# Kernel tuning notes

Hardware: AMD Instinct MI355X
Metric: run time of the kernel (lower is better)

## Reference

```python
import jax, jax.numpy as jnp
import numpy as np

N_ITEMS = 100000
EMBED_DIM = 64
N_REL = 3
N_EDGES = 3200000


def setup_inputs() -> dict:
    key = jax.random.key(0)
    k1, k2, k3, k4 = jax.random.split(key, 4)
    item_embeddings = jax.random.normal(k1, (N_ITEMS, EMBED_DIM), dtype=jnp.float32)
    rows = jax.random.randint(k2, (N_REL, N_EDGES), 0, N_ITEMS, dtype=jnp.int64)
    cols = jax.random.randint(k3, (N_REL, N_EDGES), 0, N_ITEMS, dtype=jnp.int64)
    vals = jax.random.uniform(k4, (N_REL, N_EDGES), dtype=jnp.float32)
    return {"item_embeddings": item_embeddings, "rows": rows, "cols": cols, "vals": vals}


def reference(item_embeddings, rows, cols, vals):
    # item_embeddings: [N, D]; rows/cols/vals: [R, E] COO edge lists per relation.
    n_items, _ = item_embeddings.shape
    n_rel = rows.shape[0]
    rel_emb = jnp.zeros_like(item_embeddings)
    for r in range(n_rel):  # fixed small number of relation types
        # SpMM: neighbor_emb[i] = sum_{e: rows[e]==i} vals[e] * E[cols[e]]
        msgs = item_embeddings[cols[r]] * vals[r][:, None]          # [E, D]
        neighbor = jax.ops.segment_sum(msgs, rows[r], num_segments=n_items)  # [N, D]
        # degree = row sum of adjacency values, clamped to min 1
        degree = jax.ops.segment_sum(vals[r], rows[r], num_segments=n_items)  # [N]
        degree = jnp.maximum(degree, 1.0)
        rel_emb = rel_emb + neighbor / degree[:, None]
    rel_emb = rel_emb / n_rel
    return item_embeddings + rel_emb
```

## Files before the change

kernel.cpp:

```cpp
#include <hip/hip_runtime.h>

#define N_ITEMS     100000
#define EMBED_DIM   64
#define N_REL       3
#define N_EDGES     3200000
#define TOTAL_EDGES (N_REL * N_EDGES)
#define NKEY        (N_REL * N_ITEMS)

#define LOG_CH   6
#define CH_ROWS  64
#define NCHUNK   1563
#define NBKT     (NCHUNK * N_REL)
#define BCAP     2368
#define LOG_CB   12
#define NCB      25
#define TILEP    4096
#define SEGSB    34
#define CBCAP    (SEGSB * TILEP)
#define NTILEA   ((N_EDGES + TILEP - 1) / TILEP)

__global__ void initall_kernel(unsigned* __restrict__ gcursorF,
                               unsigned* __restrict__ cursorC) {
    int i = blockIdx.x * 256 + threadIdx.x;
    if (i < NBKT) gcursorF[i] = (unsigned)i * (unsigned)BCAP;
    if (i < N_REL * NCB) cursorC[i] = (unsigned)(i % NCB) * (unsigned)CBCAP;
}

__global__ void tobf16_kernel(const float* __restrict__ E, unsigned short* __restrict__ Ebf) {
    int i = blockIdx.x * 256 + threadIdx.x;
    if (i < N_ITEMS * EMBED_DIM) {
        unsigned u = __float_as_uint(E[i]);
        unsigned r = (u + 0x7FFFu + ((u >> 16) & 1u)) >> 16;
        Ebf[i] = (unsigned short)r;
    }
}

__launch_bounds__(512)
__global__ void partA_kernel(const int* __restrict__ rows,
                             const int* __restrict__ cols,
                             const float* __restrict__ vals,
                             unsigned* __restrict__ cursorC,
                             uint2* __restrict__ coarse,
                             int rel) {
    __shared__ uint2 stag[TILEP];
    __shared__ unsigned char bkt[TILEP];
    __shared__ unsigned hist[NCB], lstart[NCB], gbase[NCB], lcur[NCB];
    int base = blockIdx.x * TILEP;
    int cnt = N_EDGES - base; if (cnt > TILEP) cnt = TILEP;
    int t = threadIdx.x;
    const int go = rel * N_EDGES + base;

    if (t < NCB) hist[t] = 0u;
    __syncthreads();
    for (int i = t; i < cnt; i += 512)
        atomicAdd(&hist[(unsigned)rows[go + i] >> LOG_CB], 1u);
    __syncthreads();
    if (t == 0) {
        unsigned run = 0;
        for (int j = 0; j < NCB; j++) { unsigned v = hist[j]; lstart[j] = run; lcur[j] = run; run += v; }
    }
    __syncthreads();
    if (t < NCB && hist[t]) gbase[t] = atomicAdd(&cursorC[rel * NCB + t], hist[t]);
    __syncthreads();
    for (int i = t; i < cnt; i += 512) {
        unsigned row = (unsigned)rows[go + i];
        unsigned cb = row >> LOG_CB;
        unsigned dst = atomicAdd(&lcur[cb], 1u);
        stag[dst] = make_uint2((unsigned)cols[go + i] | ((row & 4095u) << 17),
                               __float_as_uint(vals[go + i]));
        bkt[dst] = (unsigned char)cb;
    }
    __syncthreads();
    for (int i = t; i < cnt; i += 512) {
        unsigned bb = bkt[i];
        unsigned dst = gbase[bb] + ((unsigned)i - lstart[bb]);
        if (dst < (bb + 1u) * (unsigned)CBCAP) coarse[dst] = stag[i];
    }
}

__launch_bounds__(512)
__global__ void partB_kernel(const unsigned* __restrict__ cursorC,
                             const uint2* __restrict__ coarse,
                             unsigned* __restrict__ gcursorF,
                             uint2* __restrict__ recs,
                             int rel) {
    __shared__ uint2 stag[TILEP];
    __shared__ unsigned char bkt[TILEP];
    __shared__ unsigned hist[64], lstart[64], gbase[64], lcur[64];
    int cb = blockIdx.x / SEGSB, seg = blockIdx.x % SEGSB;
    unsigned cntA = cursorC[rel * NCB + cb] - (unsigned)cb * (unsigned)CBCAP;
    if (cntA > (unsigned)CBCAP) cntA = (unsigned)CBCAP;
    int off = seg * TILEP;
    int cnt = (int)cntA - off;
    if (cnt <= 0) return;
    if (cnt > TILEP) cnt = TILEP;
    const uint2* __restrict__ src = coarse + (unsigned)cb * (unsigned)CBCAP + off;
    int t = threadIdx.x;

    if (t < 64) hist[t] = 0u;
    __syncthreads();
    for (int i = t; i < cnt; i += 512)
        atomicAdd(&hist[(src[i].x >> 23) & 63u], 1u);
    __syncthreads();
    if (t == 0) {
        unsigned run = 0;
        for (int j = 0; j < 64; j++) { unsigned v = hist[j]; lstart[j] = run; lcur[j] = run; run += v; }
    }
    __syncthreads();
    if (t < 64 && hist[t])
        gbase[t] = atomicAdd(&gcursorF[(((unsigned)cb << 6) + t) * 3u + rel], hist[t]);
    __syncthreads();
    for (int i = t; i < cnt; i += 512) {
        uint2 rc = src[i];
        unsigned j = (rc.x >> 23) & 63u;
        unsigned dst = atomicAdd(&lcur[j], 1u);
        stag[dst] = make_uint2(rc.x & 0x7FFFFFu, rc.y);
        bkt[dst] = (unsigned char)j;
    }
    __syncthreads();
    for (int i = t; i < cnt; i += 512) {
        unsigned j = bkt[i];
        unsigned bf = (((unsigned)cb << 6) + j) * 3u + rel;
        unsigned dst = gbase[j] + ((unsigned)i - lstart[j]);
        if (dst < (bf + 1u) * (unsigned)BCAP) recs[dst] = stag[i];
    }
}

__launch_bounds__(512, 8)
__global__ void gather_sort_kernel(const uint2* __restrict__ Ebf4,
                                   const float* __restrict__ E,
                                   const unsigned* __restrict__ gcursorF,
                                   const uint2* __restrict__ recs,
                                   float* __restrict__ out) {
    __shared__ uint2  srt[BCAP];
    __shared__ float4 accT4[CH_ROWS * 16];
    __shared__ unsigned hist[CH_ROWS], cur[CH_ROWS], rstart[CH_ROWS + 1];
    int c = blockIdx.x;
    int t = threadIdx.x;
    int w = t >> 6;
    int lane = t & 63;
    int sub = lane >> 4;
    int q = lane & 15;

    float* accT = (float*)accT4;
    for (int k = t; k < CH_ROWS * EMBED_DIM; k += 512) accT[k] = 0.f;

    for (int rel = 0; rel < N_REL; rel++) {
        unsigned b = (unsigned)(c * N_REL + rel);
        unsigned s0 = b * (unsigned)BCAP;
        int n = (int)(gcursorF[b] - s0);
        if (n > BCAP) n = BCAP;
        const uint2* __restrict__ pg = recs + s0;

        uint2 rc[5];
        #pragma unroll
        for (int k = 0; k < 5; k++) {
            int i = t + (k << 9);
            rc[k] = (i < n) ? pg[i] : make_uint2(0u, 0u);
        }
        if (t < CH_ROWS) hist[t] = 0u;
        __syncthreads();
        #pragma unroll
        for (int k = 0; k < 5; k++) {
            int i = t + (k << 9);
            if (i < n) atomicAdd(&hist[rc[k].x >> 17], 1u);
        }
        __syncthreads();
        if (t < 64) {
            unsigned v = hist[t];
            unsigned inc = v;
            #pragma unroll
            for (int d = 1; d < 64; d <<= 1) {
                unsigned x = __shfl_up(inc, d, 64);
                if (lane >= d) inc += x;
            }
            rstart[t] = inc - v;
            cur[t] = inc - v;
            if (t == 63) rstart[64] = inc;
        }
        __syncthreads();
        #pragma unroll
        for (int k = 0; k < 5; k++) {
            int i = t + (k << 9);
            if (i < n) {
                unsigned pos = atomicAdd(&cur[rc[k].x >> 17], 1u);
                srt[pos] = make_uint2(rc[k].x & 0x1FFFFu, rc[k].y);
            }
        }
        __syncthreads();

        for (int k = 0; k < 8; k++) {
            int r = (w << 3) + k;
            int base = (int)rstart[r];
            int nr = (int)(rstart[r + 1] - rstart[r]);
            float a0 = 0.f, a1 = 0.f, a2 = 0.f, a3 = 0.f, dg = 0.f;
            int i = sub;
            for (; i + 12 < nr; i += 16) {
                uint2 r0 = srt[base + i],     r1 = srt[base + i + 4];
                uint2 r2 = srt[base + i + 8], r3 = srt[base + i + 12];
                uint2 e0 = Ebf4[r0.x * 16u + q];
                uint2 e1 = Ebf4[r1.x * 16u + q];
                uint2 e2 = Ebf4[r2.x * 16u + q];
                uint2 e3 = Ebf4[r3.x * 16u + q];
                float w0 = __uint_as_float(r0.y), w1 = __uint_as_float(r1.y);
                float w2 = __uint_as_float(r2.y), w3 = __uint_as_float(r3.y);
                a0 += w0 * __uint_as_float(e0.x << 16);
                a1 += w0 * __uint_as_float(e0.x & 0xFFFF0000u);
                a2 += w0 * __uint_as_float(e0.y << 16);
                a3 += w0 * __uint_as_float(e0.y & 0xFFFF0000u);
                dg += w0;
                a0 += w1 * __uint_as_float(e1.x << 16);
                a1 += w1 * __uint_as_float(e1.x & 0xFFFF0000u);
                a2 += w1 * __uint_as_float(e1.y << 16);
                a3 += w1 * __uint_as_float(e1.y & 0xFFFF0000u);
                dg += w1;
                a0 += w2 * __uint_as_float(e2.x << 16);
                a1 += w2 * __uint_as_float(e2.x & 0xFFFF0000u);
                a2 += w2 * __uint_as_float(e2.y << 16);
                a3 += w2 * __uint_as_float(e2.y & 0xFFFF0000u);
                dg += w2;
                a0 += w3 * __uint_as_float(e3.x << 16);
                a1 += w3 * __uint_as_float(e3.x & 0xFFFF0000u);
                a2 += w3 * __uint_as_float(e3.y << 16);
                a3 += w3 * __uint_as_float(e3.y & 0xFFFF0000u);
                dg += w3;
            }
            for (; i < nr; i += 4) {
                uint2 r0 = srt[base + i];
                uint2 e0 = Ebf4[r0.x * 16u + q];
                float w0 = __uint_as_float(r0.y);
                a0 += w0 * __uint_as_float(e0.x << 16);
                a1 += w0 * __uint_as_float(e0.x & 0xFFFF0000u);
                a2 += w0 * __uint_as_float(e0.y << 16);
                a3 += w0 * __uint_as_float(e0.y & 0xFFFF0000u);
                dg += w0;
            }
            a0 += __shfl_xor(a0, 16, 64);  a0 += __shfl_xor(a0, 32, 64);
            a1 += __shfl_xor(a1, 16, 64);  a1 += __shfl_xor(a1, 32, 64);
            a2 += __shfl_xor(a2, 16, 64);  a2 += __shfl_xor(a2, 32, 64);
            a3 += __shfl_xor(a3, 16, 64);  a3 += __shfl_xor(a3, 32, 64);
            dg += __shfl_xor(dg, 16, 64);  dg += __shfl_xor(dg, 32, 64);
            float inv = 1.0f / (3.0f * fmaxf(dg, 1.0f));
            if (sub == 0) {
                float4 o = accT4[(r << 4) + q];
                accT4[(r << 4) + q] = make_float4(o.x + a0 * inv, o.y + a1 * inv,
                                                  o.z + a2 * inv, o.w + a3 * inv);
            }
        }
        __syncthreads();
    }

    int gbase2 = c * (CH_ROWS * EMBED_DIM);
    for (int k = t; k < CH_ROWS * EMBED_DIM; k += 512) {
        int gi = gbase2 + k;
        if (gi < N_ITEMS * EMBED_DIM) out[gi] = E[gi] + accT[k];
    }
}

__global__ void binscatter_cap_kernel(const int* __restrict__ rows,
                                      const int* __restrict__ cols,
                                      const float* __restrict__ vals,
                                      unsigned* __restrict__ gcursor,
                                      uint2* __restrict__ recs) {
    int stride = gridDim.x * blockDim.x;
    for (int i = blockIdx.x * blockDim.x + threadIdx.x; i < TOTAL_EDGES; i += stride) {
        unsigned rel = (unsigned)i / (unsigned)N_EDGES;
        unsigned row = (unsigned)rows[i];
        unsigned b = (row >> LOG_CH) * 3u + rel;
        unsigned pos = atomicAdd(&gcursor[b], 1u);
        if (pos < (b + 1u) * (unsigned)BCAP)
            recs[pos] = make_uint2((unsigned)cols[i] | ((row & (unsigned)(CH_ROWS - 1)) << 17),
                                   __float_as_uint(vals[i]));
    }
}

#define NBS ((NKEY + 255) / 256)

__global__ void hist300_kernel(const int* __restrict__ rows, unsigned* __restrict__ cnt) {
    int stride = gridDim.x * blockDim.x;
    for (int i = blockIdx.x * blockDim.x + threadIdx.x; i < TOTAL_EDGES; i += stride) {
        unsigned r = (unsigned)i / (unsigned)N_EDGES;
        unsigned key = r * N_ITEMS + (unsigned)rows[i];
        atomicAdd(&cnt[key], 1u);
    }
}

__global__ void scan_blocksum(const unsigned* __restrict__ cnt, unsigned* __restrict__ bsum) {
    __shared__ unsigned s[256];
    int i = blockIdx.x * 256 + threadIdx.x;
    s[threadIdx.x] = (i < NKEY) ? cnt[i] : 0u;
    __syncthreads();
    for (int off = 128; off > 0; off >>= 1) {
        if (threadIdx.x < off) s[threadIdx.x] += s[threadIdx.x + off];
        __syncthreads();
    }
    if (threadIdx.x == 0) bsum[blockIdx.x] = s[0];
}

__global__ void scan_partials(unsigned* __restrict__ bsum, unsigned* __restrict__ starts) {
    const int IT = 5;
    int t = threadIdx.x;
    unsigned loc[IT];
    unsigned sum = 0;
    #pragma unroll
    for (int k = 0; k < IT; k++) {
        int idx = t * IT + k;
        loc[k] = (idx < NBS) ? bsum[idx] : 0u;
        sum += loc[k];
    }
    int lane = t & 63, wid = t >> 6;
    unsigned inc = sum;
    #pragma unroll
    for (int d = 1; d < 64; d <<= 1) {
        unsigned x = __shfl_up(inc, d, 64);
        if (lane >= d) inc += x;
    }
    __shared__ unsigned woff[4], woffEx[4];
    if (lane == 63) woff[wid] = inc;
    __syncthreads();
    if (t == 0) { unsigned run = 0; for (int k = 0; k < 4; k++) { woffEx[k] = run; run += woff[k]; } }
    __syncthreads();
    unsigned ex = inc - sum + woffEx[wid];
    #pragma unroll
    for (int k = 0; k < IT; k++) {
        int idx = t * IT + k;
        if (idx < NBS) { bsum[idx] = ex; ex += loc[k]; }
    }
    if (t == 0) starts[NKEY] = (unsigned)TOTAL_EDGES;
}

__global__ void scan_final(unsigned* key_arr,
                           const unsigned* __restrict__ bsum,
                           unsigned* __restrict__ cursor) {
    int i = blockIdx.x * 256 + threadIdx.x;
    unsigned v = (i < NKEY) ? key_arr[i] : 0u;
    int lane = threadIdx.x & 63, wid = threadIdx.x >> 6;
    unsigned inc = v;
    #pragma unroll
    for (int d = 1; d < 64; d <<= 1) {
        unsigned x = __shfl_up(inc, d, 64);
        if (lane >= d) inc += x;
    }
    __shared__ unsigned woff[4], woffEx[4];
    if (lane == 63) woff[wid] = inc;
    __syncthreads();
    if (threadIdx.x == 0) { unsigned run = 0; for (int k = 0; k < 4; k++) { woffEx[k] = run; run += woff[k]; } }
    __syncthreads();
    unsigned ex = inc - v + woffEx[wid] + bsum[blockIdx.x];
    if (i < NKEY) { key_arr[i] = ex; cursor[i] = ex; }
}

__global__ void binscatter2_kernel(const int* __restrict__ rows,
                                   const int* __restrict__ cols,
                                   const float* __restrict__ vals,
                                   unsigned* __restrict__ cursor,
                                   uint2* __restrict__ recs) {
    int stride = gridDim.x * blockDim.x;
    for (int i = blockIdx.x * blockDim.x + threadIdx.x; i < TOTAL_EDGES; i += stride) {
        unsigned r = (unsigned)i / (unsigned)N_EDGES;
        unsigned key = r * N_ITEMS + (unsigned)rows[i];
        unsigned pos = atomicAdd(&cursor[key], 1u);
        uint2 rec;
        rec.x = (unsigned)cols[i];
        rec.y = __float_as_uint(vals[i]);
        recs[pos] = rec;
    }
}

__launch_bounds__(192)
__global__ void gather_csr_f32_kernel(const float* __restrict__ E,
                                      const unsigned* __restrict__ starts,
                                      const uint2* __restrict__ recs,
                                      float* __restrict__ out) {
    __shared__ float part[N_REL * EMBED_DIM];
    int row = blockIdx.x;
    int w = threadIdx.x >> 6;
    int d = threadIdx.x & 63;
    unsigned key = (unsigned)w * N_ITEMS + (unsigned)row;
    unsigned s = starts[key];
    int n = (int)(starts[key + 1] - s);
    const uint2* __restrict__ p = recs + s;
    float acc = 0.0f, deg = 0.0f;
    int j = 0;
    for (; j + 8 <= n; j += 8) {
        uint2 a[8];
        #pragma unroll
        for (int k = 0; k < 8; k++) a[k] = p[j + k];
        float e[8];
        #pragma unroll
        for (int k = 0; k < 8; k++) e[k] = E[a[k].x * EMBED_DIM + d];
        #pragma unroll
        for (int k = 0; k < 8; k++) {
            float wv = __uint_as_float(a[k].y);
            acc += wv * e[k];
            deg += wv;
        }
    }
    for (; j < n; j++) {
        uint2 a = p[j];
        float wv = __uint_as_float(a.y);
        acc += wv * E[a.x * EMBED_DIM + d];
        deg += wv;
    }
    part[w * EMBED_DIM + d] = acc / (3.0f * fmaxf(deg, 1.0f));
    __syncthreads();
    if (threadIdx.x < EMBED_DIM) {
        int gi = row * EMBED_DIM + threadIdx.x;
        out[gi] = E[gi] + part[threadIdx.x]
                        + part[EMBED_DIM + threadIdx.x]
                        + part[2 * EMBED_DIM + threadIdx.x];
    }
}

__global__ void deg_kernel(const int* __restrict__ rows,
                           const float* __restrict__ vals,
                           float* __restrict__ deg) {
    long long i = (long long)blockIdx.x * blockDim.x + threadIdx.x;
    if (i >= TOTAL_EDGES) return;
    int r = (int)(i / N_EDGES);
    int row = rows[i];
    atomicAdd(&deg[(long long)r * N_ITEMS + row], vals[i]);
}

__global__ void inv_kernel(float* __restrict__ deg) {
    int i = blockIdx.x * blockDim.x + threadIdx.x;
    if (i >= N_REL * N_ITEMS) return;
    float d = deg[i];
    d = fmaxf(d, 1.0f);
    deg[i] = 1.0f / (3.0f * d);
}

__global__ void scatter_kernel(const float* __restrict__ E,
                               const int* __restrict__ rows,
                               const int* __restrict__ cols,
                               const float* __restrict__ vals,
                               const float* __restrict__ inv,
                               float* __restrict__ out) {
    long long t = (long long)blockIdx.x * blockDim.x + threadIdx.x;
    long long edge = t >> 6;
    int d = (int)(t & 63);
    if (edge >= TOTAL_EDGES) return;
    int r = (int)(edge / N_EDGES);
    int row = rows[edge];
    int col = cols[edge];
    float w = vals[edge] * inv[r * N_ITEMS + row];
    float msg = w * E[(long long)col * EMBED_DIM + d];
    atomicAdd(&out[(long long)row * EMBED_DIM + d], msg);
}

extern "C" void kernel_launch(void* const* d_in, const int* in_sizes, int n_in,
                              void* d_out, int out_size, void* d_ws, size_t ws_size,
                              hipStream_t stream) {
    const float* E    = (const float*)d_in[0];
    const int*   rows = (const int*)d_in[1];
    const int*   cols = (const int*)d_in[2];
    const float* vals = (const float*)d_in[3];
    float* out = (float*)d_out;

    const size_t GCB      = 32768;
    const size_t COARSE_B = (size_t)NCB * CBCAP * sizeof(uint2);
    const size_t FINE_B   = (size_t)NBKT * BCAP * sizeof(uint2);
    const size_t EBF_B    = (size_t)N_ITEMS * EMBED_DIM * 2;
    size_t need11 = GCB + COARSE_B + FINE_B + EBF_B;
    size_t need10 = GCB + FINE_B + EBF_B;

    const size_t REGA = 1204224;
    const size_t REGC = 8192;
    const size_t RECB = (size_t)TOTAL_EDGES * sizeof(uint2);
    size_t need5 = 2 * REGA + REGC + RECB;

    if (ws_size >= need11) {
        unsigned* gcursorF = (unsigned*)d_ws;
        unsigned* cursorC  = (unsigned*)((char*)d_ws + 20480);
        uint2*    coarse   = (uint2*)((char*)d_ws + GCB);
        uint2*    recs     = (uint2*)((char*)d_ws + GCB + COARSE_B);
        unsigned short* Ebf = (unsigned short*)((char*)d_ws + GCB + COARSE_B + FINE_B);

        initall_kernel<<<(NBKT + 255) / 256, 256, 0, stream>>>(gcursorF, cursorC);
        tobf16_kernel<<<(N_ITEMS * EMBED_DIM + 255) / 256, 256, 0, stream>>>(E, Ebf);
        for (int r = 0; r < N_REL; r++) {
            partA_kernel<<<NTILEA, 512, 0, stream>>>(rows, cols, vals, cursorC, coarse, r);
            partB_kernel<<<NCB * SEGSB, 512, 0, stream>>>(cursorC, coarse, gcursorF, recs, r);
        }
        gather_sort_kernel<<<NCHUNK, 512, 0, stream>>>((const uint2*)Ebf, E, gcursorF, recs, out);
    } else if (ws_size >= need10) {
        unsigned* gcursorF = (unsigned*)d_ws;
        unsigned* cursorC  = (unsigned*)((char*)d_ws + 20480);
        uint2*    recs     = (uint2*)((char*)d_ws + GCB);
        unsigned short* Ebf = (unsigned short*)((char*)d_ws + GCB + FINE_B);

        initall_kernel<<<(NBKT + 255) / 256, 256, 0, stream>>>(gcursorF, cursorC);
        tobf16_kernel<<<(N_ITEMS * EMBED_DIM + 255) / 256, 256, 0, stream>>>(E, Ebf);
        binscatter_cap_kernel<<<2048, 256, 0, stream>>>(rows, cols, vals, gcursorF, recs);
        gather_sort_kernel<<<NCHUNK, 512, 0, stream>>>((const uint2*)Ebf, E, gcursorF, recs, out);
    } else if (ws_size >= need5) {
        unsigned* keyA   = (unsigned*)d_ws;
        unsigned* cursor = (unsigned*)((char*)d_ws + REGA);
        unsigned* bsum   = (unsigned*)((char*)d_ws + 2 * REGA);
        uint2*    recs   = (uint2*)((char*)d_ws + 2 * REGA + REGC);

        hipMemsetAsync(keyA, 0, NKEY * sizeof(unsigned), stream);
        hist300_kernel<<<1536, 256, 0, stream>>>(rows, keyA);
        scan_blocksum<<<NBS, 256, 0, stream>>>(keyA, bsum);
        scan_partials<<<1, 256, 0, stream>>>(bsum, keyA);
        scan_final<<<NBS, 256, 0, stream>>>(keyA, bsum, cursor);
        binscatter2_kernel<<<2048, 256, 0, stream>>>(rows, cols, vals, cursor, recs);
        gather_csr_f32_kernel<<<N_ITEMS, 192, 0, stream>>>(E, keyA, recs, out);
    } else {
        float* deg = (float*)d_ws;
        hipMemsetAsync(deg, 0, (size_t)N_REL * N_ITEMS * sizeof(float), stream);
        {
            long long total = TOTAL_EDGES;
            int block = 256;
            long long grid = (total + block - 1) / block;
            deg_kernel<<<(unsigned)grid, block, 0, stream>>>(rows, vals, deg);
        }
        {
            int total = N_REL * N_ITEMS;
            int block = 256;
            int grid = (total + block - 1) / block;
            inv_kernel<<<grid, block, 0, stream>>>(deg);
        }
        hipMemcpyAsync(out, E, (size_t)N_ITEMS * EMBED_DIM * sizeof(float),
                       hipMemcpyDeviceToDevice, stream);
        {
            long long threads = (long long)TOTAL_EDGES * 64;
            int block = 256;
            long long grid = (threads + block - 1) / block;
            scatter_kernel<<<(unsigned)grid, block, 0, stream>>>(E, rows, cols, vals, deg, out);
        }
    }
}
```

Measured before the change: 440.1 us.

## Batch all relations into single partition launches with register-staged edges and warp scans

Adds per-relation coarse buffers so both partition passes run all three relations in one launch each, replacing six serialized launches with two. It halves the tile size so each thread holds its edges in registers, loading them once instead of twice. The serial single-thread prefix scan over bucket histograms is replaced by a wavefront shuffle scan. In exchange the workspace need grows by two more coarse buffers, and a fallback path keeps the per-relation loop when workspace is too small.

```diff
diff --git a/kernel.cpp b/kernel.cpp
--- a/kernel.cpp
+++ b/kernel.cpp
@@ -14,10 +14,10 @@
 #define BCAP     2368
 #define LOG_CB   12
 #define NCB      25
-#define TILEP    4096
-#define SEGSB    34
+#define TILEP    2048
+#define NTILEP   ((N_EDGES + TILEP - 1) / TILEP)
+#define SEGSB    68
 #define CBCAP    (SEGSB * TILEP)
-#define NTILEA   ((N_EDGES + TILEP - 1) / TILEP)
 
 __global__ void initall_kernel(unsigned* __restrict__ gcursorF,
                                unsigned* __restrict__ cursorC) {
@@ -36,87 +36,125 @@
 }
 
 __launch_bounds__(512)
-__global__ void partA_kernel(const int* __restrict__ rows,
-                             const int* __restrict__ cols,
-                             const float* __restrict__ vals,
-                             unsigned* __restrict__ cursorC,
-                             uint2* __restrict__ coarse,
-                             int rel) {
+__global__ void partA2_kernel(const int* __restrict__ rows,
+                              const int* __restrict__ cols,
+                              const float* __restrict__ vals,
+                              unsigned* __restrict__ cursorC,
+                              uint2* __restrict__ coarse,
+                              int rel0, unsigned relStrideU2) {
     __shared__ uint2 stag[TILEP];
     __shared__ unsigned char bkt[TILEP];
     __shared__ unsigned hist[NCB], lstart[NCB], gbase[NCB], lcur[NCB];
-    int base = blockIdx.x * TILEP;
+    int rel = rel0 + blockIdx.x / NTILEP;
+    int base = (blockIdx.x % NTILEP) * TILEP;
     int cnt = N_EDGES - base; if (cnt > TILEP) cnt = TILEP;
     int t = threadIdx.x;
     const int go = rel * N_EDGES + base;
-
+    uint2* __restrict__ coarseRel = coarse + (size_t)(rel - rel0) * relStrideU2;
+
+    unsigned rrow[4], rcol[4], rval[4];
+    #pragma unroll
+    for (int k = 0; k < 4; k++) {
+        int i = t + (k << 9);
+        if (i < cnt) {
+            rrow[k] = (unsigned)rows[go + i];
+            rcol[k] = (unsigned)cols[go + i];
+            rval[k] = __float_as_uint(vals[go + i]);
+        } else rrow[k] = 0xFFFFFFFFu;
+    }
     if (t < NCB) hist[t] = 0u;
     __syncthreads();
-    for (int i = t; i < cnt; i += 512)
-        atomicAdd(&hist[(unsigned)rows[go + i] >> LOG_CB], 1u);
-    __syncthreads();
-    if (t == 0) {
-        unsigned run = 0;
-        for (int j = 0; j < NCB; j++) { unsigned v = hist[j]; lstart[j] = run; lcur[j] = run; run += v; }
-    }
-    __syncthreads();
-    if (t < NCB && hist[t]) gbase[t] = atomicAdd(&cursorC[rel * NCB + t], hist[t]);
-    __syncthreads();
-    for (int i = t; i < cnt; i += 512) {
-        unsigned row = (unsigned)rows[go + i];
-        unsigned cb = row >> LOG_CB;
-        unsigned dst = atomicAdd(&lcur[cb], 1u);
-        stag[dst] = make_uint2((unsigned)cols[go + i] | ((row & 4095u) << 17),
-                               __float_as_uint(vals[go + i]));
-        bkt[dst] = (unsigned char)cb;
-    }
+    #pragma unroll
+    for (int k = 0; k < 4; k++)
+        if (rrow[k] != 0xFFFFFFFFu) atomicAdd(&hist[rrow[k] >> LOG_CB], 1u);
+    __syncthreads();
+    if (t < 32) {
+        unsigned v = (t < NCB) ? hist[t] : 0u;
+        unsigned inc = v;
+        #pragma unroll
+        for (int d = 1; d < 32; d <<= 1) {
+            unsigned x = __shfl_up(inc, d, 32);
+            if (t >= d) inc += x;
+        }
+        if (t < NCB) {
+            unsigned ex = inc - v;
+            lstart[t] = ex; lcur[t] = ex;
+            if (v) gbase[t] = atomicAdd(&cursorC[rel * NCB + t], v);
+        }
+    }
+    __syncthreads();
+    #pragma unroll
+    for (int k = 0; k < 4; k++)
+        if (rrow[k] != 0xFFFFFFFFu) {
+            unsigned row = rrow[k];
+            unsigned cb = row >> LOG_CB;
+            unsigned dst = atomicAdd(&lcur[cb], 1u);
+            stag[dst] = make_uint2(rcol[k] | ((row & 4095u) << 17), rval[k]);
+            bkt[dst] = (unsigned char)cb;
+        }
     __syncthreads();
     for (int i = t; i < cnt; i += 512) {
         unsigned bb = bkt[i];
         unsigned dst = gbase[bb] + ((unsigned)i - lstart[bb]);
-        if (dst < (bb + 1u) * (unsigned)CBCAP) coarse[dst] = stag[i];
+        if (dst < (bb + 1u) * (unsigned)CBCAP) coarseRel[dst] = stag[i];
     }
 }
 
 __launch_bounds__(512)
-__global__ void partB_kernel(const unsigned* __restrict__ cursorC,
-                             const uint2* __restrict__ coarse,
-                             unsigned* __restrict__ gcursorF,
-                             uint2* __restrict__ recs,
-                             int rel) {
+__global__ void partB2_kernel(const unsigned* __restrict__ cursorC,
+                              const uint2* __restrict__ coarse,
+                              unsigned* __restrict__ gcursorF,
+                              uint2* __restrict__ recs,
+                              int rel0, unsigned relStrideU2) {
     __shared__ uint2 stag[TILEP];
     __shared__ unsigned char bkt[TILEP];
     __shared__ unsigned hist[64], lstart[64], gbase[64], lcur[64];
-    int cb = blockIdx.x / SEGSB, seg = blockIdx.x % SEGSB;
+    int rel = rel0 + blockIdx.x / (NCB * SEGSB);
+    int rem = blockIdx.x % (NCB * SEGSB);
+    int cb = rem / SEGSB, seg = rem % SEGSB;
     unsigned cntA = cursorC[rel * NCB + cb] - (unsigned)cb * (unsigned)CBCAP;
     if (cntA > (unsigned)CBCAP) cntA = (unsigned)CBCAP;
     int off = seg * TILEP;
     int cnt = (int)cntA - off;
     if (cnt <= 0) return;
     if (cnt > TILEP) cnt = TILEP;
-    const uint2* __restrict__ src = coarse + (unsigned)cb * (unsigned)CBCAP + off;
+    const uint2* __restrict__ src = coarse + (size_t)(rel - rel0) * relStrideU2
+                                  + (unsigned)cb * (unsigned)CBCAP + off;
     int t = threadIdx.x;
 
+    uint2 rc[4];
+    #pragma unroll
+    for (int k = 0; k < 4; k++) {
+        int i = t + (k << 9);
+        rc[k] = (i < cnt) ? src[i] : make_uint2(0xFFFFFFFFu, 0u);
+    }
     if (t < 64) hist[t] = 0u;
     __syncthreads();
-    for (int i = t; i < cnt; i += 512)
-        atomicAdd(&hist[(src[i].x >> 23) & 63u], 1u);
-    __syncthreads();
-    if (t == 0) {
-        unsigned run = 0;
-        for (int j = 0; j < 64; j++) { unsigned v = hist[j]; lstart[j] = run; lcur[j] = run; run += v; }
-    }
-    __syncthreads();
-    if (t < 64 && hist[t])
-        gbase[t] = atomicAdd(&gcursorF[(((unsigned)cb << 6) + t) * 3u + rel], hist[t]);
-    __syncthreads();
-    for (int i = t; i < cnt; i += 512) {
-        uint2 rc = src[i];
-        unsigned j = (rc.x >> 23) & 63u;
-        unsigned dst = atomicAdd(&lcur[j], 1u);
-        stag[dst] = make_uint2(rc.x & 0x7FFFFFu, rc.y);
-        bkt[dst] = (unsigned char)j;
-    }
+    #pragma unroll
+    for (int k = 0; k < 4; k++)
+        if (rc[k].x != 0xFFFFFFFFu) atomicAdd(&hist[(rc[k].x >> 23) & 63u], 1u);
+    __syncthreads();
+    if (t < 64) {
+        unsigned v = hist[t];
+        unsigned inc = v;
+        #pragma unroll
+        for (int d = 1; d < 64; d <<= 1) {
+            unsigned x = __shfl_up(inc, d, 64);
+            if (t >= d) inc += x;
+        }
+        unsigned ex = inc - v;
+        lstart[t] = ex; lcur[t] = ex;
+        if (v) gbase[t] = atomicAdd(&gcursorF[(((unsigned)cb << 6) + t) * 3u + rel], v);
+    }
+    __syncthreads();
+    #pragma unroll
+    for (int k = 0; k < 4; k++)
+        if (rc[k].x != 0xFFFFFFFFu) {
+            unsigned j = (rc[k].x >> 23) & 63u;
+            unsigned dst = atomicAdd(&lcur[j], 1u);
+            stag[dst] = make_uint2(rc[k].x & 0x7FFFFFu, rc[k].y);
+            bkt[dst] = (unsigned char)j;
+        }
     __syncthreads();
     for (int i = t; i < cnt; i += 512) {
         unsigned j = bkt[i];
@@ -257,23 +295,6 @@
     }
 }
 
-__global__ void binscatter_cap_kernel(const int* __restrict__ rows,
-                                      const int* __restrict__ cols,
-                                      const float* __restrict__ vals,
-                                      unsigned* __restrict__ gcursor,
-                                      uint2* __restrict__ recs) {
-    int stride = gridDim.x * blockDim.x;
-    for (int i = blockIdx.x * blockDim.x + threadIdx.x; i < TOTAL_EDGES; i += stride) {
-        unsigned rel = (unsigned)i / (unsigned)N_EDGES;
-        unsigned row = (unsigned)rows[i];
-        unsigned b = (row >> LOG_CH) * 3u + rel;
-        unsigned pos = atomicAdd(&gcursor[b], 1u);
-        if (pos < (b + 1u) * (unsigned)BCAP)
-            recs[pos] = make_uint2((unsigned)cols[i] | ((row & (unsigned)(CH_ROWS - 1)) << 17),
-                                   __float_as_uint(vals[i]));
-    }
-}
-
 #define NBS ((NKEY + 255) / 256)
 
 __global__ void hist300_kernel(const int* __restrict__ rows, unsigned* __restrict__ cnt) {
@@ -458,40 +479,46 @@
     float* out = (float*)d_out;
 
     const size_t GCB      = 32768;
-    const size_t COARSE_B = (size_t)NCB * CBCAP * sizeof(uint2);
+    const size_t COARSE1  = (size_t)NCB * CBCAP * sizeof(uint2);
     const size_t FINE_B   = (size_t)NBKT * BCAP * sizeof(uint2);
     const size_t EBF_B    = (size_t)N_ITEMS * EMBED_DIM * 2;
-    size_t need11 = GCB + COARSE_B + FINE_B + EBF_B;
-    size_t need10 = GCB + FINE_B + EBF_B;
+    size_t need12 = GCB + 3 * COARSE1 + FINE_B + EBF_B;
+    size_t need11 = GCB + COARSE1 + FINE_B + EBF_B;
 
     const size_t REGA = 1204224;
     const size_t REGC = 8192;
     const size_t RECB = (size_t)TOTAL_EDGES * sizeof(uint2);
     size_t need5 = 2 * REGA + REGC + RECB;
 
-    if (ws_size >= need11) {
+    if (ws_size >= need12) {
         unsigned* gcursorF = (unsigned*)d_ws;
         unsigned* cursorC  = (unsigned*)((char*)d_ws + 20480);
         uint2*    coarse   = (uint2*)((char*)d_ws + GCB);
-        uint2*    recs     = (uint2*)((char*)d_ws + GCB + COARSE_B);
-        unsigned short* Ebf = (unsigned short*)((char*)d_ws + GCB + COARSE_B + FINE_B);
+        uint2*    recs     = (uint2*)((char*)d_ws + GCB + 3 * COARSE1);
+        unsigned short* Ebf = (unsigned short*)((char*)d_ws + GCB + 3 * COARSE1 + FINE_B);
+
+        initall_kernel<<<(NBKT + 255) / 256, 256, 0, stream>>>(gcursorF, cursorC);
+        tobf16_kernel<<<(N_ITEMS * EMBED_DIM + 255) / 256, 256, 0, stream>>>(E, Ebf);
+        partA2_kernel<<<N_REL * NTILEP, 512, 0, stream>>>(
+            rows, cols, vals, cursorC, coarse, 0, (unsigned)(NCB * CBCAP));
+        partB2_kernel<<<N_REL * NCB * SEGSB, 512, 0, stream>>>(
+            cursorC, coarse, gcursorF, recs, 0, (unsigned)(NCB * CBCAP));
+        gather_sort_kernel<<<NCHUNK, 512, 0, stream>>>((const uint2*)Ebf, E, gcursorF, recs, out);
+    } else if (ws_size >= need11) {
+        unsigned* gcursorF = (unsigned*)d_ws;
+        unsigned* cursorC  = (unsigned*)((char*)d_ws + 20480);
+        uint2*    coarse   = (uint2*)((char*)d_ws + GCB);
+        uint2*    recs     = (uint2*)((char*)d_ws + GCB + COARSE1);
+        unsigned short* Ebf = (unsigned short*)((char*)d_ws + GCB + COARSE1 + FINE_B);
 
         initall_kernel<<<(NBKT + 255) / 256, 256, 0, stream>>>(gcursorF, cursorC);
         tobf16_kernel<<<(N_ITEMS * EMBED_DIM + 255) / 256, 256, 0, stream>>>(E, Ebf);
         for (int r = 0; r < N_REL; r++) {
-            partA_kernel<<<NTILEA, 512, 0, stream>>>(rows, cols, vals, cursorC, coarse, r);
-            partB_kernel<<<NCB * SEGSB, 512, 0, stream>>>(cursorC, coarse, gcursorF, recs, r);
-        }
-        gather_sort_kernel<<<NCHUNK, 512, 0, stream>>>((const uint2*)Ebf, E, gcursorF, recs, out);
-    } else if (ws_size >= need10) {
-        unsigned* gcursorF = (unsigned*)d_ws;
-        unsigned* cursorC  = (unsigned*)((char*)d_ws + 20480);
-        uint2*    recs     = (uint2*)((char*)d_ws + GCB);
-        unsigned short* Ebf = (unsigned short*)((char*)d_ws + GCB + FINE_B);
-
-        initall_kernel<<<(NBKT + 255) / 256, 256, 0, stream>>>(gcursorF, cursorC);
-        tobf16_kernel<<<(N_ITEMS * EMBED_DIM + 255) / 256, 256, 0, stream>>>(E, Ebf);
-        binscatter_cap_kernel<<<2048, 256, 0, stream>>>(rows, cols, vals, gcursorF, recs);
+            partA2_kernel<<<NTILEP, 512, 0, stream>>>(
+                rows, cols, vals, cursorC, coarse, r, 0u);
+            partB2_kernel<<<NCB * SEGSB, 512, 0, stream>>>(
+                cursorC, coarse, gcursorF, recs, r, 0u);
+        }
         gather_sort_kernel<<<NCHUNK, 512, 0, stream>>>((const uint2*)Ebf, E, gcursorF, recs, out);
     } else if (ws_size >= need5) {
         unsigned* keyA   = (unsigned*)d_ws;
```

After: 396.3 us. 1.11x faster.
